# Performance work log

Measured on AMD Instinct MI355X. Metric: run time of the kernel, lower is better.

## Reference

```python
import jax, jax.numpy as jnp
import numpy as np


def setup_inputs() -> dict:
    key = jax.random.key(0)
    ks = jax.random.split(key, 5)
    S, B, H, L = 512, 64, 1024, 2
    scale = 0.1
    return {
        "x": jax.random.normal(ks[0], (S, B, H), dtype=jnp.float32),
        "h0": jnp.zeros((L, B, H), dtype=jnp.float32),
        "c0": jnp.zeros((L, B, H), dtype=jnp.float32),
        "Wx": jax.random.uniform(ks[1], (L, 4 * H, H), minval=-scale, maxval=scale, dtype=jnp.float32),
        "Wh": jax.random.uniform(ks[2], (L, 4 * H, H), minval=-scale, maxval=scale, dtype=jnp.float32),
        "bx": jax.random.uniform(ks[3], (L, 4 * H), minval=-scale, maxval=scale, dtype=jnp.float32),
        "bh": jax.random.uniform(ks[4], (L, 4 * H), minval=-scale, maxval=scale, dtype=jnp.float32),
    }


def _cell(x_t, h_prev, c_prev, Wx_l, Wh_l, bx_l, bh_l, H):
    # gates: [B, 4H]; chunk order per source: f, i, o, c_ex
    gates = x_t @ Wx_l.T + bx_l + h_prev @ Wh_l.T + bh_l
    f, i, o, c_ex = jnp.split(gates, 4, axis=1)
    f = jax.nn.sigmoid(f)
    i = jax.nn.sigmoid(i)
    o = jax.nn.sigmoid(o)
    c_ex = jnp.tanh(c_ex)
    c = f * c_prev + i * c_ex
    h = o * jnp.tanh(c)
    return h, c


def reference(x, h0, c0, Wx, Wh, bx, bh):
    # x: [S, B, H]; h0/c0: [L, B, H]; Wx/Wh: [L, 4H, H]; bx/bh: [L, 4H]
    L = h0.shape[0]
    H = h0.shape[-1]

    def step(carry, x_t):
        h_all, c_all = carry  # each [L, B, H]
        out = x_t
        hs, cs = [], []
        for l in range(L):  # small fixed layer count
            h, c = _cell(out, h_all[l], c_all[l], Wx[l], Wh[l], bx[l], bh[l], H)
            out = h  # dropout is identity in eval mode
            hs.append(h)
            cs.append(c)
        return (jnp.stack(hs, 0), jnp.stack(cs, 0)), out

    (h_fin, c_fin), ys = jax.lax.scan(step, (h0, c0), x)
    return ys, (h_fin, c_fin)
```

## Files before the change

### kernel.cpp

```cpp
#include <hip/hip_runtime.h>

typedef __bf16 bf16_t;
typedef __bf16 bf16x8 __attribute__((ext_vector_type(8)));
typedef __bf16 bf16x4 __attribute__((ext_vector_type(4)));
typedef float  f32x4  __attribute__((ext_vector_type(4)));
typedef unsigned long long u64;

#define S_LEN 512
#define BATCH 64
#define HID 1024
#define BH (BATCH*HID)
#define G4 (4*HID)
#define NBLK 256
#define LBLK 128
#define NTHR 512
#define FSTRIDE 32
#define NCNT 16
#define RSKEW 7

__device__ __forceinline__ float sigmoid_f(float x) { return 1.f / (1.f + __expf(-x)); }
__device__ __forceinline__ float tanh_f(float x) {
    float e = __expf(-2.f * fabsf(x));
    float t = (1.f - e) / (1.f + e);
    return x >= 0.f ? t : -t;
}

__device__ __forceinline__ bf16x8 cvt8(const float* p) {
    float4 a = *reinterpret_cast<const float4*>(p);
    float4 b = *reinterpret_cast<const float4*>(p + 4);
    bf16x8 r;
    r[0] = (bf16_t)a.x; r[1] = (bf16_t)a.y; r[2] = (bf16_t)a.z; r[3] = (bf16_t)a.w;
    r[4] = (bf16_t)b.x; r[5] = (bf16_t)b.y; r[6] = (bf16_t)b.z; r[7] = (bf16_t)b.w;
    return r;
}

__device__ __forceinline__ void wait_one(unsigned* cnt, int layer, unsigned thr,
                                         int tid, int lane) {
    if (tid < 64) {
        for (;;) {
            unsigned v = 0;
            if (lane < NCNT)
                v = __hip_atomic_load(&cnt[(layer * NCNT + lane) * FSTRIDE],
                                      __ATOMIC_RELAXED, __HIP_MEMORY_SCOPE_AGENT);
            unsigned s = v;
            s += __shfl_xor(s, 1);
            s += __shfl_xor(s, 2);
            s += __shfl_xor(s, 4);
            s += __shfl_xor(s, 8);
            if (__shfl(s, 0) >= thr) break;
            __builtin_amdgcn_s_sleep(1);
        }
    }
    __syncthreads();
}

__device__ __forceinline__ void wait_two_fence(unsigned* cnt, unsigned thr0, unsigned thr1,
                                               int tid, int lane) {
    if (tid < 64) {
        for (;;) {
            unsigned v = 0;
            if (lane < 2 * NCNT)
                v = __hip_atomic_load(&cnt[lane * FSTRIDE], __ATOMIC_RELAXED,
                                      __HIP_MEMORY_SCOPE_AGENT);
            unsigned s = v;
            s += __shfl_xor(s, 1);
            s += __shfl_xor(s, 2);
            s += __shfl_xor(s, 4);
            s += __shfl_xor(s, 8);
            unsigned S0 = __shfl(s, 0);
            unsigned S1 = __shfl(s, 16);
            if (S0 >= thr0 && S1 >= thr1) break;
            __builtin_amdgcn_s_sleep(1);
        }
        __builtin_amdgcn_fence(__ATOMIC_ACQUIRE, "agent");
    }
    __syncthreads();
}

__global__ void prep_kernel(const float* __restrict__ h0,
                            bf16_t* __restrict__ h0buf, bf16_t* __restrict__ h1buf,
                            unsigned* __restrict__ cnt, int mask0, int mask1) {
    int gtid = blockIdx.x * blockDim.x + threadIdx.x;
    int gsz  = gridDim.x * blockDim.x;
    if (gtid < 2 * NCNT) cnt[gtid * FSTRIDE] = 0u;
    for (int i = gtid; i < BH; i += gsz) {
        h0buf[(size_t)mask0 * BH + i] = (bf16_t)h0[i];
        h1buf[(size_t)mask1 * BH + i] = (bf16_t)h0[BH + i];
    }
}

__global__ __launch_bounds__(NTHR, 2) void lstm_persistent(
    const float* __restrict__ x,
    const float* __restrict__ c0,
    const float* __restrict__ Wx,
    const float* __restrict__ Wh,
    const float* __restrict__ bx,
    const float* __restrict__ bh,
    float* __restrict__ out,
    bf16_t* __restrict__ h0buf,
    bf16_t* __restrict__ h1buf,
    unsigned* __restrict__ cnt,
    int ff, int mask0, int mask1)
{
    __shared__ __attribute__((aligned(16))) unsigned char lds_w[256 * 512];
    __shared__ __attribute__((aligned(16))) float lds_red[8 * 256];
    __shared__ __attribute__((aligned(16))) float lds_hf[BATCH * 8];

    const int tid  = threadIdx.x;
    const int bid  = blockIdx.x;
    const int l    = bid >> 7;
    const int ug8  = bid & 127;
    const int lane = tid & 63;
    const int wv   = tid >> 6;
    const int mt   = wv >> 1;
    const int kh   = wv & 1;
    const int quad = lane >> 4;
    const int r16  = lane & 15;

    float* ys   = out;
    float* hfin = out + (size_t)S_LEN * BH;
    float* cfin = hfin + 2 * BH;

    {
        const float* WxL = Wx + (size_t)l * G4 * HID;
        const float* WhL = Wh + (size_t)l * G4 * HID;
        for (int ch = tid; ch < 32 * 256; ch += NTHR) {
            int row = ch & 31;
            int gr  = ch >> 5;
            int ul = row >> 2, g = row & 3;
            size_t R = (size_t)g * HID + 8 * ug8 + ul;
            const float* src = (gr < 128) ? (WxL + R * HID + (size_t)gr * 8)
                                          : (WhL + R * HID + (size_t)(gr - 128) * 8);
            *reinterpret_cast<bf16x8*>(&lds_w[gr * 512 + row * 16]) = cvt8(src);
        }
    }

    const int b_loc  = lane >> 2;
    const int uu     = lane & 3;
    const int b_glob = 16 * mt + b_loc;
    const int u_loc  = 4 * kh + uu;
    const int u_glob = 8 * ug8 + u_loc;

    float bias_r[4];
    #pragma unroll
    for (int gi = 0; gi < 4; ++gi) {
        int R = gi * HID + u_glob;
        bias_r[gi] = bx[l * G4 + R] + bh[l * G4 + R];
    }
    float c_reg = c0[(size_t)l * BH + (size_t)b_glob * HID + u_glob];

    bf16_t* pubbuf = (l == 0) ? h0buf : h1buf;
    const int pubmask = (l == 0) ? mask0 : mask1;
    unsigned* mycnt = &cnt[(l * NCNT + (ug8 & (NCNT - 1))) * FSTRIDE];
    __syncthreads();

    const int arow_off = (16 * mt + r16) * HID + kh * 512 + quad * 8;

    bf16x8 axp[16];
    if (l == 0) {
        const float* arow = x + arow_off;
        #pragma unroll
        for (int ks = 0; ks < 16; ++ks) axp[ks] = cvt8(arow + ks * 32);
    }

    for (int t = 0; t < S_LEN; ++t) {
        f32x4 acc0 = {0.f, 0.f, 0.f, 0.f};
        f32x4 acc1 = {0.f, 0.f, 0.f, 0.f};

        if (l == 0) {
            #pragma unroll
            for (int ks = 0; ks < 16; ++ks) {
                int gr = kh * 64 + ks * 4 + quad;
                bf16x8 b0 = *reinterpret_cast<const bf16x8*>(&lds_w[gr * 512 + r16 * 16]);
                bf16x8 b1 = *reinterpret_cast<const bf16x8*>(&lds_w[gr * 512 + (16 + r16) * 16]);
                acc0 = __builtin_amdgcn_mfma_f32_16x16x32_bf16(axp[ks], b0, acc0, 0, 0, 0);
                acc1 = __builtin_amdgcn_mfma_f32_16x16x32_bf16(axp[ks], b1, acc1, 0, 0, 0);
            }
            if (ff) {
                wait_one(cnt, 0, (unsigned)(LBLK * t), tid, lane);
            } else {
                unsigned thr1 = (t > RSKEW) ? (unsigned)(LBLK * (t - RSKEW)) : 0u;
                wait_two_fence(cnt, (unsigned)(LBLK * t), thr1, tid, lane);
            }
            const bf16_t* ah = h0buf + (size_t)((t - 1) & mask0) * BH + arow_off;
            bf16x8 af[16];
            #pragma unroll
            for (int ks = 0; ks < 16; ++ks)
                af[ks] = *reinterpret_cast<const bf16x8*>(ah + ks * 32);
            #pragma unroll
            for (int ks = 0; ks < 16; ++ks) {
                int gr = 128 + kh * 64 + ks * 4 + quad;
                bf16x8 b0 = *reinterpret_cast<const bf16x8*>(&lds_w[gr * 512 + r16 * 16]);
                bf16x8 b1 = *reinterpret_cast<const bf16x8*>(&lds_w[gr * 512 + (16 + r16) * 16]);
                acc0 = __builtin_amdgcn_mfma_f32_16x16x32_bf16(af[ks], b0, acc0, 0, 0, 0);
                acc1 = __builtin_amdgcn_mfma_f32_16x16x32_bf16(af[ks], b1, acc1, 0, 0, 0);
            }
        } else {
            if (ff) {
                wait_one(cnt, 0, (unsigned)(LBLK * (t + 1)), tid, lane);
                const bf16_t* ax = h0buf + (size_t)(t & mask0) * BH + arow_off;
                bf16x8 axf[16];
                #pragma unroll
                for (int ks = 0; ks < 16; ++ks)
                    axf[ks] = *reinterpret_cast<const bf16x8*>(ax + ks * 32);
                #pragma unroll
                for (int ks = 0; ks < 16; ++ks) {
                    int gr = kh * 64 + ks * 4 + quad;
                    bf16x8 b0 = *reinterpret_cast<const bf16x8*>(&lds_w[gr * 512 + r16 * 16]);
                    bf16x8 b1 = *reinterpret_cast<const bf16x8*>(&lds_w[gr * 512 + (16 + r16) * 16]);
                    acc0 = __builtin_amdgcn_mfma_f32_16x16x32_bf16(axf[ks], b0, acc0, 0, 0, 0);
                    acc1 = __builtin_amdgcn_mfma_f32_16x16x32_bf16(axf[ks], b1, acc1, 0, 0, 0);
                }
                wait_one(cnt, 1, (unsigned)(LBLK * t), tid, lane);
                const bf16_t* ah = h1buf + (size_t)((t - 1) & mask1) * BH + arow_off;
                bf16x8 ahf[16];
                #pragma unroll
                for (int ks = 0; ks < 16; ++ks)
                    ahf[ks] = *reinterpret_cast<const bf16x8*>(ah + ks * 32);
                #pragma unroll
                for (int ks = 0; ks < 16; ++ks) {
                    int gr = 128 + kh * 64 + ks * 4 + quad;
                    bf16x8 b0 = *reinterpret_cast<const bf16x8*>(&lds_w[gr * 512 + r16 * 16]);
                    bf16x8 b1 = *reinterpret_cast<const bf16x8*>(&lds_w[gr * 512 + (16 + r16) * 16]);
                    acc0 = __builtin_amdgcn_mfma_f32_16x16x32_bf16(ahf[ks], b0, acc0, 0, 0, 0);
                    acc1 = __builtin_amdgcn_mfma_f32_16x16x32_bf16(ahf[ks], b1, acc1, 0, 0, 0);
                }
            } else {
                wait_two_fence(cnt, (unsigned)(LBLK * (t + 1)), (unsigned)(LBLK * t), tid, lane);
                const bf16_t* ax = h0buf + (size_t)(t & mask0) * BH + arow_off;
                const bf16_t* ah = h1buf + (size_t)((t - 1) & mask1) * BH + arow_off;
                bf16x8 axf[16], ahf[16];
                #pragma unroll
                for (int ks = 0; ks < 16; ++ks)
                    axf[ks] = *reinterpret_cast<const bf16x8*>(ax + ks * 32);
                #pragma unroll
                for (int ks = 0; ks < 16; ++ks)
                    ahf[ks] = *reinterpret_cast<const bf16x8*>(ah + ks * 32);
                #pragma unroll
                for (int ks = 0; ks < 16; ++ks) {
                    int gr = kh * 64 + ks * 4 + quad;
                    bf16x8 b0 = *reinterpret_cast<const bf16x8*>(&lds_w[gr * 512 + r16 * 16]);
                    bf16x8 b1 = *reinterpret_cast<const bf16x8*>(&lds_w[gr * 512 + (16 + r16) * 16]);
                    acc0 = __builtin_amdgcn_mfma_f32_16x16x32_bf16(axf[ks], b0, acc0, 0, 0, 0);
                    acc1 = __builtin_amdgcn_mfma_f32_16x16x32_bf16(axf[ks], b1, acc1, 0, 0, 0);
                }
                #pragma unroll
                for (int ks = 0; ks < 16; ++ks) {
                    int gr = 128 + kh * 64 + ks * 4 + quad;
                    bf16x8 b0 = *reinterpret_cast<const bf16x8*>(&lds_w[gr * 512 + r16 * 16]);
                    bf16x8 b1 = *reinterpret_cast<const bf16x8*>(&lds_w[gr * 512 + (16 + r16) * 16]);
                    acc0 = __builtin_amdgcn_mfma_f32_16x16x32_bf16(ahf[ks], b0, acc0, 0, 0, 0);
                    acc1 = __builtin_amdgcn_mfma_f32_16x16x32_bf16(ahf[ks], b1, acc1, 0, 0, 0);
                }
            }
        }

        {
            f32x4 ship = kh ? acc0 : acc1;
            *reinterpret_cast<f32x4*>(&lds_red[wv * 256 + lane * 4]) = ship;
            __syncthreads();
            f32x4 part = *reinterpret_cast<const f32x4*>(&lds_red[(wv ^ 1) * 256 + lane * 4]);
            f32x4 keep = kh ? acc1 : acc0;
            acc0 = keep + part;
        }

        {
            const int quad_s = b_loc >> 2;
            const int reg_s  = b_loc & 3;
            float gsum[4];
            #pragma unroll
            for (int gi = 0; gi < 4; ++gi) {
                int lane_s = (quad_s << 4) | (4 * uu + gi);
                float v0 = __shfl(acc0[0], lane_s, 64);
                float v1 = __shfl(acc0[1], lane_s, 64);
                float v2 = __shfl(acc0[2], lane_s, 64);
                float v3 = __shfl(acc0[3], lane_s, 64);
                float v  = (reg_s == 0) ? v0 : (reg_s == 1) ? v1 : (reg_s == 2) ? v2 : v3;
                gsum[gi] = v + bias_r[gi];
            }
            float fg = sigmoid_f(gsum[0]);
            float ig = sigmoid_f(gsum[1]);
            float og = sigmoid_f(gsum[2]);
            float cx = tanh_f(gsum[3]);
            float cN = fg * c_reg + ig * cx;
            float h  = og * tanh_f(cN);
            c_reg = cN;
            lds_hf[b_glob * 8 + u_loc] = h;
            if (t == S_LEN - 1) {
                hfin[(size_t)l * BH + (size_t)b_glob * HID + u_glob] = h;
                cfin[(size_t)l * BH + (size_t)b_glob * HID + u_glob] = cN;
            }
        }
        __syncthreads();

        if (tid < 64) {
            const float* hp = &lds_hf[lane * 8];
            union { bf16x4 v; u64 q; } p0, p1;
            #pragma unroll
            for (int j = 0; j < 4; ++j) {
                p0.v[j] = (bf16_t)hp[j];
                p1.v[j] = (bf16_t)hp[4 + j];
            }
            bf16_t* dst = pubbuf + (size_t)(t & pubmask) * BH + (size_t)lane * HID + 8 * ug8;
            __hip_atomic_store((u64*)(void*)dst,       p0.q, __ATOMIC_RELAXED, __HIP_MEMORY_SCOPE_AGENT);
            __hip_atomic_store((u64*)(void*)(dst + 4), p1.q, __ATOMIC_RELAXED, __HIP_MEMORY_SCOPE_AGENT);
            asm volatile("s_waitcnt vmcnt(0)" ::: "memory");
            if (lane == 0) atomicAdd(mycnt, 1u);
            if (l == 1) {
                float* yd = ys + (size_t)t * BH + (size_t)lane * HID + 8 * ug8;
                __builtin_nontemporal_store(*reinterpret_cast<const f32x4*>(hp),     reinterpret_cast<f32x4*>(yd));
                __builtin_nontemporal_store(*reinterpret_cast<const f32x4*>(hp + 4), reinterpret_cast<f32x4*>(yd + 4));
            }
        }

        if (l == 0 && t + 1 < S_LEN) {
            const float* arow = x + (size_t)(t + 1) * BH + arow_off;
            #pragma unroll
            for (int ks = 0; ks < 16; ++ks) axp[ks] = cvt8(arow + ks * 32);
        }
    }
}

extern "C" void kernel_launch(void* const* d_in, const int* in_sizes, int n_in,
                              void* d_out, int out_size, void* d_ws, size_t ws_size,
                              hipStream_t stream) {
    (void)in_sizes; (void)n_in; (void)out_size;
    const float* x  = (const float*)d_in[0];
    const float* h0 = (const float*)d_in[1];
    const float* c0 = (const float*)d_in[2];
    const float* Wx = (const float*)d_in[3];
    const float* Wh = (const float*)d_in[4];
    const float* bx = (const float*)d_in[5];
    const float* bh = (const float*)d_in[6];

    unsigned char* ws = (unsigned char*)d_ws;
    unsigned* cnt = (unsigned*)ws;
    size_t off = 32768;
    size_t need_ff = off + (size_t)2 * S_LEN * BH * 2;
    int ff, mask0, mask1;
    bf16_t *h0buf, *h1buf;
    if (ws_size >= need_ff) {
        ff = 1; mask0 = S_LEN - 1; mask1 = S_LEN - 1;
        h0buf = (bf16_t*)(ws + off); off += (size_t)S_LEN * BH * 2;
        h1buf = (bf16_t*)(ws + off);
    } else {
        ff = 0; mask0 = 7; mask1 = 1;
        h0buf = (bf16_t*)(ws + off); off += (size_t)8 * BH * 2;
        h1buf = (bf16_t*)(ws + off);
    }

    prep_kernel<<<2048, 256, 0, stream>>>(h0, h0buf, h1buf, cnt, mask0, mask1);
    lstm_persistent<<<NBLK, NTHR, 0, stream>>>(x, c0, Wx, Wh, bx, bh, (float*)d_out,
                                               h0buf, h1buf, cnt, ff, mask0, mask1);
}
```

Measured before the change: 6.661 ms.

## Replace global step barrier with per-chunk counters and streamed chunked GEMM waits

Inter-block synchronisation moves from one summed barrier over all producer blocks to per-chunk counters, one per group of 16 producer blocks covering 128 hidden columns. Each wave waits only on the chunks its K slice needs, in order, and double-buffers the h loads so MFMAs on one chunk overlap the wait and load for the next. The layer-0 skew throttle against layer 1 moves to the publish point, and the counter increment becomes a relaxed agent-scope fetch_add. This is meant to cut barrier latency on the serial recurrence, at the cost of more atomic polling traffic and per-wave spin loops with no block-wide barrier.

```diff
diff --git a/kernel.cpp b/kernel.cpp
--- a/kernel.cpp
+++ b/kernel.cpp
@@ -14,9 +14,8 @@
 #define NBLK 256
 #define LBLK 128
 #define NTHR 512
-#define FSTRIDE 32
-#define NCNT 16
-#define RSKEW 7
+#define CSTRIDE 32
+#define NCHK 8
 
 __device__ __forceinline__ float sigmoid_f(float x) { return 1.f / (1.f + __expf(-x)); }
 __device__ __forceinline__ float tanh_f(float x) {
@@ -34,47 +33,45 @@
     return r;
 }
 
-__device__ __forceinline__ void wait_one(unsigned* cnt, int layer, unsigned thr,
-                                         int tid, int lane) {
-    if (tid < 64) {
-        for (;;) {
-            unsigned v = 0;
-            if (lane < NCNT)
-                v = __hip_atomic_load(&cnt[(layer * NCNT + lane) * FSTRIDE],
-                                      __ATOMIC_RELAXED, __HIP_MEMORY_SCOPE_AGENT);
-            unsigned s = v;
-            s += __shfl_xor(s, 1);
-            s += __shfl_xor(s, 2);
-            s += __shfl_xor(s, 4);
-            s += __shfl_xor(s, 8);
-            if (__shfl(s, 0) >= thr) break;
-            __builtin_amdgcn_s_sleep(1);
-        }
-    }
-    __syncthreads();
-}
-
-__device__ __forceinline__ void wait_two_fence(unsigned* cnt, unsigned thr0, unsigned thr1,
-                                               int tid, int lane) {
-    if (tid < 64) {
-        for (;;) {
-            unsigned v = 0;
-            if (lane < 2 * NCNT)
-                v = __hip_atomic_load(&cnt[lane * FSTRIDE], __ATOMIC_RELAXED,
-                                      __HIP_MEMORY_SCOPE_AGENT);
-            unsigned s = v;
-            s += __shfl_xor(s, 1);
-            s += __shfl_xor(s, 2);
-            s += __shfl_xor(s, 4);
-            s += __shfl_xor(s, 8);
-            unsigned S0 = __shfl(s, 0);
-            unsigned S1 = __shfl(s, 16);
-            if (S0 >= thr0 && S1 >= thr1) break;
-            __builtin_amdgcn_s_sleep(1);
-        }
-        __builtin_amdgcn_fence(__ATOMIC_ACQUIRE, "agent");
-    }
-    __syncthreads();
+__device__ __forceinline__ void wait_chunk(const unsigned* cp, unsigned thr) {
+    if (__hip_atomic_load(cp, __ATOMIC_RELAXED, __HIP_MEMORY_SCOPE_AGENT) < thr) {
+        do { __builtin_amdgcn_s_sleep(2); }
+        while (__hip_atomic_load(cp, __ATOMIC_RELAXED, __HIP_MEMORY_SCOPE_AGENT) < thr);
+    }
+    asm volatile("" ::: "memory");
+}
+
+__device__ __forceinline__ void gemm_phase_chunked(
+    const bf16_t* __restrict__ abase, const unsigned* __restrict__ cbase, unsigned thr,
+    int grbase, const unsigned char* __restrict__ lds_w,
+    int kh, int quad, int r16, int ff, f32x4& acc0, f32x4& acc1)
+{
+    bf16x8 af[8];
+    wait_chunk(&cbase[(4 * kh) * CSTRIDE], thr);
+    if (!ff) __builtin_amdgcn_fence(__ATOMIC_ACQUIRE, "agent");
+    #pragma unroll
+    for (int j = 0; j < 4; ++j)
+        af[j] = *reinterpret_cast<const bf16x8*>(abase + j * 32);
+    #pragma unroll
+    for (int c = 0; c < 4; ++c) {
+        if (c < 3) {
+            wait_chunk(&cbase[(4 * kh + c + 1) * CSTRIDE], thr);
+            if (!ff) __builtin_amdgcn_fence(__ATOMIC_ACQUIRE, "agent");
+            #pragma unroll
+            for (int j = 0; j < 4; ++j)
+                af[((c + 1) & 1) * 4 + j] =
+                    *reinterpret_cast<const bf16x8*>(abase + (4 * (c + 1) + j) * 32);
+        }
+        #pragma unroll
+        for (int j = 0; j < 4; ++j) {
+            int ks = 4 * c + j;
+            int gr = grbase + kh * 64 + ks * 4 + quad;
+            bf16x8 b0 = *reinterpret_cast<const bf16x8*>(&lds_w[gr * 512 + r16 * 16]);
+            bf16x8 b1 = *reinterpret_cast<const bf16x8*>(&lds_w[gr * 512 + (16 + r16) * 16]);
+            acc0 = __builtin_amdgcn_mfma_f32_16x16x32_bf16(af[(c & 1) * 4 + j], b0, acc0, 0, 0, 0);
+            acc1 = __builtin_amdgcn_mfma_f32_16x16x32_bf16(af[(c & 1) * 4 + j], b1, acc1, 0, 0, 0);
+        }
+    }
 }
 
 __global__ void prep_kernel(const float* __restrict__ h0,
@@ -82,7 +79,7 @@
                             unsigned* __restrict__ cnt, int mask0, int mask1) {
     int gtid = blockIdx.x * blockDim.x + threadIdx.x;
     int gsz  = gridDim.x * blockDim.x;
-    if (gtid < 2 * NCNT) cnt[gtid * FSTRIDE] = 0u;
+    if (gtid < 2 * NCHK) cnt[gtid * CSTRIDE] = 0u;
     for (int i = gtid; i < BH; i += gsz) {
         h0buf[(size_t)mask0 * BH + i] = (bf16_t)h0[i];
         h1buf[(size_t)mask1 * BH + i] = (bf16_t)h0[BH + i];
@@ -151,7 +148,9 @@
 
     bf16_t* pubbuf = (l == 0) ? h0buf : h1buf;
     const int pubmask = (l == 0) ? mask0 : mask1;
-    unsigned* mycnt = &cnt[(l * NCNT + (ug8 & (NCNT - 1))) * FSTRIDE];
+    const unsigned* cnt0 = cnt;
+    const unsigned* cnt1 = cnt + NCHK * CSTRIDE;
+    unsigned* mycnt = &cnt[(l * NCHK + (ug8 >> 4)) * CSTRIDE];
     __syncthreads();
 
     const int arow_off = (16 * mt + r16) * HID + kh * 512 + quad * 8;
@@ -176,83 +175,16 @@
                 acc0 = __builtin_amdgcn_mfma_f32_16x16x32_bf16(axp[ks], b0, acc0, 0, 0, 0);
                 acc1 = __builtin_amdgcn_mfma_f32_16x16x32_bf16(axp[ks], b1, acc1, 0, 0, 0);
             }
-            if (ff) {
-                wait_one(cnt, 0, (unsigned)(LBLK * t), tid, lane);
-            } else {
-                unsigned thr1 = (t > RSKEW) ? (unsigned)(LBLK * (t - RSKEW)) : 0u;
-                wait_two_fence(cnt, (unsigned)(LBLK * t), thr1, tid, lane);
-            }
             const bf16_t* ah = h0buf + (size_t)((t - 1) & mask0) * BH + arow_off;
-            bf16x8 af[16];
-            #pragma unroll
-            for (int ks = 0; ks < 16; ++ks)
-                af[ks] = *reinterpret_cast<const bf16x8*>(ah + ks * 32);
-            #pragma unroll
-            for (int ks = 0; ks < 16; ++ks) {
-                int gr = 128 + kh * 64 + ks * 4 + quad;
-                bf16x8 b0 = *reinterpret_cast<const bf16x8*>(&lds_w[gr * 512 + r16 * 16]);
-                bf16x8 b1 = *reinterpret_cast<const bf16x8*>(&lds_w[gr * 512 + (16 + r16) * 16]);
-                acc0 = __builtin_amdgcn_mfma_f32_16x16x32_bf16(af[ks], b0, acc0, 0, 0, 0);
-                acc1 = __builtin_amdgcn_mfma_f32_16x16x32_bf16(af[ks], b1, acc1, 0, 0, 0);
-            }
+            gemm_phase_chunked(ah, cnt0, (unsigned)(16 * t), 128, lds_w,
+                               kh, quad, r16, ff, acc0, acc1);
         } else {
-            if (ff) {
-                wait_one(cnt, 0, (unsigned)(LBLK * (t + 1)), tid, lane);
-                const bf16_t* ax = h0buf + (size_t)(t & mask0) * BH + arow_off;
-                bf16x8 axf[16];
-                #pragma unroll
-                for (int ks = 0; ks < 16; ++ks)
-                    axf[ks] = *reinterpret_cast<const bf16x8*>(ax + ks * 32);
-                #pragma unroll
-                for (int ks = 0; ks < 16; ++ks) {
-                    int gr = kh * 64 + ks * 4 + quad;
-                    bf16x8 b0 = *reinterpret_cast<const bf16x8*>(&lds_w[gr * 512 + r16 * 16]);
-                    bf16x8 b1 = *reinterpret_cast<const bf16x8*>(&lds_w[gr * 512 + (16 + r16) * 16]);
-                    acc0 = __builtin_amdgcn_mfma_f32_16x16x32_bf16(axf[ks], b0, acc0, 0, 0, 0);
-                    acc1 = __builtin_amdgcn_mfma_f32_16x16x32_bf16(axf[ks], b1, acc1, 0, 0, 0);
-                }
-                wait_one(cnt, 1, (unsigned)(LBLK * t), tid, lane);
-                const bf16_t* ah = h1buf + (size_t)((t - 1) & mask1) * BH + arow_off;
-                bf16x8 ahf[16];
-                #pragma unroll
-                for (int ks = 0; ks < 16; ++ks)
-                    ahf[ks] = *reinterpret_cast<const bf16x8*>(ah + ks * 32);
-                #pragma unroll
-                for (int ks = 0; ks < 16; ++ks) {
-                    int gr = 128 + kh * 64 + ks * 4 + quad;
-                    bf16x8 b0 = *reinterpret_cast<const bf16x8*>(&lds_w[gr * 512 + r16 * 16]);
-                    bf16x8 b1 = *reinterpret_cast<const bf16x8*>(&lds_w[gr * 512 + (16 + r16) * 16]);
-                    acc0 = __builtin_amdgcn_mfma_f32_16x16x32_bf16(ahf[ks], b0, acc0, 0, 0, 0);
-                    acc1 = __builtin_amdgcn_mfma_f32_16x16x32_bf16(ahf[ks], b1, acc1, 0, 0, 0);
-                }
-            } else {
-                wait_two_fence(cnt, (unsigned)(LBLK * (t + 1)), (unsigned)(LBLK * t), tid, lane);
-                const bf16_t* ax = h0buf + (size_t)(t & mask0) * BH + arow_off;
-                const bf16_t* ah = h1buf + (size_t)((t - 1) & mask1) * BH + arow_off;
-                bf16x8 axf[16], ahf[16];
-                #pragma unroll
-                for (int ks = 0; ks < 16; ++ks)
-                    axf[ks] = *reinterpret_cast<const bf16x8*>(ax + ks * 32);
-                #pragma unroll
-                for (int ks = 0; ks < 16; ++ks)
-                    ahf[ks] = *reinterpret_cast<const bf16x8*>(ah + ks * 32);
-                #pragma unroll
-                for (int ks = 0; ks < 16; ++ks) {
-                    int gr = kh * 64 + ks * 4 + quad;
-                    bf16x8 b0 = *reinterpret_cast<const bf16x8*>(&lds_w[gr * 512 + r16 * 16]);
-                    bf16x8 b1 = *reinterpret_cast<const bf16x8*>(&lds_w[gr * 512 + (16 + r16) * 16]);
-                    acc0 = __builtin_amdgcn_mfma_f32_16x16x32_bf16(axf[ks], b0, acc0, 0, 0, 0);
-                    acc1 = __builtin_amdgcn_mfma_f32_16x16x32_bf16(axf[ks], b1, acc1, 0, 0, 0);
-                }
-                #pragma unroll
-                for (int ks = 0; ks < 16; ++ks) {
-                    int gr = 128 + kh * 64 + ks * 4 + quad;
-                    bf16x8 b0 = *reinterpret_cast<const bf16x8*>(&lds_w[gr * 512 + r16 * 16]);
-                    bf16x8 b1 = *reinterpret_cast<const bf16x8*>(&lds_w[gr * 512 + (16 + r16) * 16]);
-                    acc0 = __builtin_amdgcn_mfma_f32_16x16x32_bf16(ahf[ks], b0, acc0, 0, 0, 0);
-                    acc1 = __builtin_amdgcn_mfma_f32_16x16x32_bf16(ahf[ks], b1, acc1, 0, 0, 0);
-                }
-            }
+            const bf16_t* ax = h0buf + (size_t)(t & mask0) * BH + arow_off;
+            gemm_phase_chunked(ax, cnt0, (unsigned)(16 * (t + 1)), 0, lds_w,
+                               kh, quad, r16, ff, acc0, acc1);
+            const bf16_t* ah = h1buf + (size_t)((t - 1) & mask1) * BH + arow_off;
+            gemm_phase_chunked(ah, cnt1, (unsigned)(16 * t), 128, lds_w,
+                               kh, quad, r16, ff, acc0, acc1);
         }
 
         {
@@ -294,6 +226,11 @@
         __syncthreads();
 
         if (tid < 64) {
+            if (!ff && l == 0 && t >= 8) {
+                #pragma unroll
+                for (int c = 0; c < NCHK; ++c)
+                    wait_chunk(&cnt1[c * CSTRIDE], (unsigned)(16 * (t - 6)));
+            }
             const float* hp = &lds_hf[lane * 8];
             union { bf16x4 v; u64 q; } p0, p1;
             #pragma unroll
@@ -305,7 +242,8 @@
             __hip_atomic_store((u64*)(void*)dst,       p0.q, __ATOMIC_RELAXED, __HIP_MEMORY_SCOPE_AGENT);
             __hip_atomic_store((u64*)(void*)(dst + 4), p1.q, __ATOMIC_RELAXED, __HIP_MEMORY_SCOPE_AGENT);
             asm volatile("s_waitcnt vmcnt(0)" ::: "memory");
-            if (lane == 0) atomicAdd(mycnt, 1u);
+            if (lane == 0)
+                __hip_atomic_fetch_add(mycnt, 1u, __ATOMIC_RELAXED, __HIP_MEMORY_SCOPE_AGENT);
             if (l == 1) {
                 float* yd = ys + (size_t)t * BH + (size_t)lane * HID + 8 * ug8;
                 __builtin_nontemporal_store(*reinterpret_cast<const f32x4*>(hp),     reinterpret_cast<f32x4*>(yd));
```

Measured after the change: 6.419 ms. 1.04x faster.
